# Kernel optimization log

Measured on AMD Instinct MI355X. Metric: run time of the kernel, lower is better.

Reference implementation:

```python
import jax, jax.numpy as jnp
import numpy as np

NUM_GROUPS = 32
EPS = 1e-6
HEAD = 8


def group_norm(x, gamma, beta):
    # x: (b, c, h, w); normalize per group of channels over (c/g, h, w)
    b, c, h, w = x.shape
    g = NUM_GROUPS
    xg = x.reshape(b, g, c // g, h, w)
    mean = xg.mean(axis=(2, 3, 4), keepdims=True)
    var = xg.var(axis=(2, 3, 4), keepdims=True)
    xn = ((xg - mean) * jax.lax.rsqrt(var + EPS)).reshape(b, c, h, w)
    return xn * gamma[None, :, None, None] + beta[None, :, None, None]


def setup_inputs() -> dict:
    key = jax.random.key(0)
    ks = jax.random.split(key, 6)
    b, c, h, w = 8, 512, 64, 64
    sd = 1.0 / np.sqrt(c)
    return {
        "x": jax.random.normal(ks[0], (b, c, h, w), jnp.float32),
        "gamma": jnp.ones((c,), jnp.float32),
        "beta": jnp.zeros((c,), jnp.float32),
        "Wq": jax.random.normal(ks[1], (c, c), jnp.float32) * sd,
        "Wk": jax.random.normal(ks[2], (c, c), jnp.float32) * sd,
        "Wv": jax.random.normal(ks[3], (c, c), jnp.float32) * sd,
        "Wp": jax.random.normal(ks[4], (c, c), jnp.float32) * sd,
        "bp": jnp.zeros((c,), jnp.float32),
    }


def reference(x, gamma, beta, Wq, Wk, Wv, Wp, bp):
    b, c, h, w = x.shape
    hd = c // HEAD
    scale = jnp.sqrt(jnp.float32(hd))  # NOTE: original MULTIPLIES by sqrt(d)
    xn = group_norm(x, gamma, beta)            # (b, c, h, w)
    x_ = xn.reshape(b, c, h * w).transpose(0, 2, 1)  # (b, n, c), n = h*w
    # torch Linear: y = x @ W.T
    Q = (x_ @ Wq.T).reshape(b, h * w, HEAD, hd)
    K = (x_ @ Wk.T).reshape(b, h * w, HEAD, hd)
    V = (x_ @ Wv.T).reshape(b, h * w, HEAD, hd)
    # einsum 'bhid,bhjd->bhij' with axes (b, n, head, hd): per-position head gram
    dots = jnp.einsum('bnid,bnjd->bnij', Q, K) * scale  # (b, n, head, head)
    att = jax.nn.softmax(dots, axis=1)  # softmax over the SPATIAL axis (dim=1)
    out = jnp.einsum('bnij,bnjd->bnid', att, V).reshape(b, h * w, c)
    out = out @ Wp.T + bp  # dropout is identity at inference
    return out.transpose(0, 2, 1).reshape(b, c, h, w) + xn  # residual adds normed x
```

## Files before the change

kernel.cpp:

```cpp
#include <hip/hip_runtime.h>
#include <stdint.h>

typedef unsigned short ushort_t;
typedef _Float16 half8 __attribute__((ext_vector_type(8)));
typedef float f32x4 __attribute__((ext_vector_type(4)));

#define GLOBAL_AS __attribute__((address_space(1)))
#define LDS_AS    __attribute__((address_space(3)))

__device__ __forceinline__ float bf2f(ushort_t u) {
    union { unsigned i; float f; } v; v.i = ((unsigned)u) << 16; return v.f;
}
__device__ __forceinline__ ushort_t f2h(float f) {
    union { _Float16 h; ushort_t u; } v; v.h = (_Float16)f; return v.u;
}
__device__ __forceinline__ float h2f(ushort_t u) {
    union { _Float16 h; ushort_t u; } v; v.u = u; return (float)v.h;
}

__device__ __forceinline__ void async16(const void* g, void* l) {
    __builtin_amdgcn_global_load_lds((const GLOBAL_AS uint32_t*)g,
                                     (LDS_AS uint32_t*)l, 16, 0, 0);
}

__device__ __forceinline__ int is_bf16_in(const uint32_t* g32) {
    return *g32 == 0x3F803F80u;
}

__global__ __launch_bounds__(256) void vecconv(const void* g, const void* be, const void* bp,
                                               float* gcan, float* bcan, float* bpcan,
                                               const uint32_t* g32) {
    int t = threadIdx.x + blockIdx.x * 256;
    if (is_bf16_in(g32)) {
        gcan[t]  = bf2f(((const ushort_t*)g)[t]);
        bcan[t]  = bf2f(((const ushort_t*)be)[t]);
        bpcan[t] = bf2f(((const ushort_t*)bp)[t]);
    } else {
        gcan[t]  = ((const float*)g)[t];
        bcan[t]  = ((const float*)be)[t];
        bpcan[t] = ((const float*)bp)[t];
    }
}

__global__ __launch_bounds__(256) void wconv(const void* Wq, const void* Wk,
                                             const void* Wv, const void* Wp,
                                             ushort_t* Wh, const uint32_t* g32) {
    const void* src = (blockIdx.y == 0) ? Wq : (blockIdx.y == 1) ? Wk
                    : (blockIdx.y == 2) ? Wv : Wp;
    ushort_t* dst = Wh + (size_t)blockIdx.y * 262144;
    const int e0 = blockIdx.x * 2048 + threadIdx.x * 8;
    ushort_t o[8];
    if (is_bf16_in(g32)) {
        uint4 u = *(const uint4*)((const ushort_t*)src + e0);
        const ushort_t* e = (const ushort_t*)&u;
#pragma unroll
        for (int j = 0; j < 8; ++j) o[j] = f2h(bf2f(e[j]));
    } else {
        float4 a = *(const float4*)((const float*)src + e0);
        float4 b = *(const float4*)((const float*)src + e0 + 4);
        o[0] = f2h(a.x); o[1] = f2h(a.y); o[2] = f2h(a.z); o[3] = f2h(a.w);
        o[4] = f2h(b.x); o[5] = f2h(b.y); o[6] = f2h(b.z); o[7] = f2h(b.w);
    }
    *(uint4*)(dst + e0) = *(const uint4*)o;
}

__global__ __launch_bounds__(256) void gn_part(const void* xv, float* __restrict__ psums,
                                               const uint32_t* g32) {
    const int bx = blockIdx.x, t = threadIdx.x;
    const size_t base = (size_t)(bx >> 3) * 65536 + (size_t)(bx & 7) * 8192;
    float s = 0.f, sq = 0.f;
    if (is_bf16_in(g32)) {
        const ushort_t* p = (const ushort_t*)xv + base;
        for (int i = 0; i < 4; ++i) {
            uint4 u = ((const uint4*)p)[t + 256 * i];
            const ushort_t* e = (const ushort_t*)&u;
#pragma unroll
            for (int j = 0; j < 8; ++j) { float f = bf2f(e[j]); s += f; sq += f * f; }
        }
    } else {
        const float* p = (const float*)xv + base;
        for (int i = 0; i < 8; ++i) {
            float4 v = ((const float4*)p)[t + 256 * i];
            s += v.x + v.y + v.z + v.w;
            sq += v.x * v.x + v.y * v.y + v.z * v.z + v.w * v.w;
        }
    }
    __shared__ float ls[256], lq[256];
    ls[t] = s; lq[t] = sq;
    __syncthreads();
    for (int off = 128; off > 0; off >>= 1) {
        if (t < off) { ls[t] += ls[t + off]; lq[t] += lq[t + off]; }
        __syncthreads();
    }
    if (t == 0) { psums[bx * 2] = ls[0]; psums[bx * 2 + 1] = lq[0]; }
}

__global__ __launch_bounds__(256) void gn_fin(const float* __restrict__ psums,
                                              float* __restrict__ stats) {
    const int t = threadIdx.x;
    float s = 0.f, q = 0.f;
#pragma unroll
    for (int k = 0; k < 8; ++k) { s += psums[(t * 8 + k) * 2]; q += psums[(t * 8 + k) * 2 + 1]; }
    float mean = s * (1.f / 65536.f);
    float var  = q * (1.f / 65536.f) - mean * mean;
    stats[t * 2 + 0] = mean;
    stats[t * 2 + 1] = rsqrtf(fmaxf(var, 0.f) + 1e-6f);
}

__global__ __launch_bounds__(256) void gn_apply_t(const void* xv,
                                                  const float* __restrict__ gcan,
                                                  const float* __restrict__ bcan,
                                                  const float* __restrict__ stats,
                                                  ushort_t* __restrict__ xnt,
                                                  const uint32_t* g32) {
    const int nt = blockIdx.x;
    const int ct = blockIdx.y;
    const int b  = blockIdx.z;
    const int t  = threadIdx.x;
    const int c0 = ct * 64, n0 = nt * 64;
    __shared__ __align__(16) ushort_t tile[64 * 80];
    if (is_bf16_in(g32)) {
        const ushort_t* x = (const ushort_t*)xv;
#pragma unroll
        for (int p = 0; p < 2; ++p) {
            int u = p * 256 + t;
            int cc = u >> 3, nc = u & 7;
            int c = c0 + cc;
            uint4 raw = *(const uint4*)(x + ((size_t)(b * 512 + c)) * 4096 + n0 + nc * 8);
            float mean = stats[(b * 32 + (c >> 4)) * 2 + 0];
            float rstd = stats[(b * 32 + (c >> 4)) * 2 + 1];
            float sc = rstd * gcan[c];
            float sh = bcan[c] - mean * sc;
            const ushort_t* e = (const ushort_t*)&raw;
#pragma unroll
            for (int j = 0; j < 8; ++j)
                tile[(nc * 8 + j) * 80 + cc] = f2h(bf2f(e[j]) * sc + sh);
        }
    } else {
        const float* x = (const float*)xv;
#pragma unroll
        for (int p = 0; p < 4; ++p) {
            int u = p * 256 + t;
            int cc = u >> 4, nc = u & 15;
            int c = c0 + cc;
            float4 raw = *(const float4*)(x + ((size_t)(b * 512 + c)) * 4096 + n0 + nc * 4);
            float mean = stats[(b * 32 + (c >> 4)) * 2 + 0];
            float rstd = stats[(b * 32 + (c >> 4)) * 2 + 1];
            float sc = rstd * gcan[c];
            float sh = bcan[c] - mean * sc;
            tile[(nc * 4 + 0) * 80 + cc] = f2h(raw.x * sc + sh);
            tile[(nc * 4 + 1) * 80 + cc] = f2h(raw.y * sc + sh);
            tile[(nc * 4 + 2) * 80 + cc] = f2h(raw.z * sc + sh);
            tile[(nc * 4 + 3) * 80 + cc] = f2h(raw.w * sc + sh);
        }
    }
    __syncthreads();
#pragma unroll
    for (int p = 0; p < 2; ++p) {
        int u = p * 256 + t;
        int nn = u >> 3, cchunk = u & 7;
        uint4 o = *(const uint4*)(tile + nn * 80 + cchunk * 8);
        *(uint4*)(xnt + ((size_t)(b * 4096 + n0 + nn)) * 512 + c0 + cchunk * 8) = o;
    }
}

__device__ __forceinline__ void gemm128_core(const ushort_t* __restrict__ A,
                                             const ushort_t* __restrict__ B,
                                             int m0, int n0, int K, f32x4 acc[4][4]) {
    __shared__ __align__(16) ushort_t As[128 * 32];
    __shared__ __align__(16) ushort_t Bs[128 * 32];
    const int t = threadIdx.x;
    const int l = t & 63;
    const int w = t >> 6;
    const int wm = (w >> 1) * 64, wn = (w & 1) * 64;
    const int lr = l & 15, q = l >> 4;
    f32x4 zero = {0.f, 0.f, 0.f, 0.f};
#pragma unroll
    for (int mi = 0; mi < 4; ++mi)
#pragma unroll
        for (int ni = 0; ni < 4; ++ni) acc[mi][ni] = zero;

    for (int kt = 0; kt < K; kt += 32) {
        __syncthreads();
#pragma unroll
        for (int p = 0; p < 2; ++p) {
            int s = p * 256 + t;
            int r = s >> 2, kc = s & 3;
            async16(A + (size_t)(m0 + r) * K + kt + kc * 8, (char*)As + p * 4096 + w * 1024);
            async16(B + (size_t)(n0 + r) * K + kt + kc * 8, (char*)Bs + p * 4096 + w * 1024);
        }
        __syncthreads();
        half8 af[4], bf[4];
#pragma unroll
        for (int mi = 0; mi < 4; ++mi)
            af[mi] = *(const half8*)(As + (wm + mi * 16 + lr) * 32 + q * 8);
#pragma unroll
        for (int ni = 0; ni < 4; ++ni)
            bf[ni] = *(const half8*)(Bs + (wn + ni * 16 + lr) * 32 + q * 8);
#pragma unroll
        for (int mi = 0; mi < 4; ++mi)
#pragma unroll
            for (int ni = 0; ni < 4; ++ni)
                acc[mi][ni] = __builtin_amdgcn_mfma_f32_16x16x32_f16(af[mi], bf[ni],
                                                                    acc[mi][ni], 0, 0, 0);
    }
}

__global__ __launch_bounds__(256) void gemm_qkv(const ushort_t* __restrict__ xnt,
                                                const ushort_t* __restrict__ Wh,
                                                ushort_t* __restrict__ Qo,
                                                ushort_t* __restrict__ Ko,
                                                ushort_t* __restrict__ Vo) {
    const int n0 = blockIdx.x * 128;
    const int m0 = blockIdx.y * 128;
    const int z  = blockIdx.z;
    const ushort_t* B = Wh + (size_t)z * 262144;
    ushort_t* C = (z == 0) ? Qo : (z == 1) ? Ko : Vo;
    f32x4 acc[4][4];
    gemm128_core(xnt, B, m0, n0, 512, acc);
    const int t = threadIdx.x, l = t & 63, w = t >> 6;
    const int wm = (w >> 1) * 64, wn = (w & 1) * 64;
    const int col = l & 15, q = l >> 4;
#pragma unroll
    for (int mi = 0; mi < 4; ++mi)
#pragma unroll
        for (int ni = 0; ni < 4; ++ni)
#pragma unroll
            for (int r = 0; r < 4; ++r) {
                int row = wm + mi * 16 + q * 4 + r;
                int cc  = wn + ni * 16 + col;
                C[(size_t)(m0 + row) * 512 + n0 + cc] = f2h(acc[mi][ni][r]);
            }
}

__global__ __launch_bounds__(256) void dots_k(const ushort_t* __restrict__ Q,
                                              const ushort_t* __restrict__ K,
                                              float* __restrict__ dots) {
    const int t = threadIdx.x, l = t & 63, w = t >> 6;
    const int gp0 = blockIdx.x * 8 + w * 2;
    const int m = l & 15, q = l >> 4;
    const size_t base = (size_t)(gp0 + (m >> 3)) * 512 + (m & 7) * 64 + q * 8;
    half8 a0 = *(const half8*)(Q + base);
    half8 a1 = *(const half8*)(Q + base + 32);
    half8 b0 = *(const half8*)(K + base);
    half8 b1 = *(const half8*)(K + base + 32);
    f32x4 acc = {0.f, 0.f, 0.f, 0.f};
    acc = __builtin_amdgcn_mfma_f32_16x16x32_f16(a0, b0, acc, 0, 0, 0);
    acc = __builtin_amdgcn_mfma_f32_16x16x32_f16(a1, b1, acc, 0, 0, 0);
    const int col = l & 15;
#pragma unroll
    for (int r = 0; r < 4; ++r) {
        int row = q * 4 + r;
        if (row < 8 && col < 8)
            dots[(size_t)gp0 * 64 + row * 8 + col] = acc[r] * 8.0f;
        if (row >= 8 && col >= 8)
            dots[(size_t)(gp0 + 1) * 64 + (row - 8) * 8 + (col - 8)] = acc[r] * 8.0f;
    }
}

__global__ __launch_bounds__(256) void smax_part(const float* __restrict__ dots,
                                                 float* __restrict__ pmax,
                                                 float* __restrict__ psum) {
    const int chunk = blockIdx.x;
    const int t = threadIdx.x;
    const int ij = t & 63, sub = t >> 6;
    const size_t base = ((size_t)chunk * 128 + sub * 32) * 64 + ij;
    float v[32];
    float m = -1e30f;
#pragma unroll
    for (int r = 0; r < 32; ++r) { v[r] = dots[base + (size_t)r * 64]; m = fmaxf(m, v[r]); }
    __shared__ float lm[4][64];
    __shared__ float lsum[4][64];
    lm[sub][ij] = m;
    __syncthreads();
    float cm = fmaxf(fmaxf(lm[0][ij], lm[1][ij]), fmaxf(lm[2][ij], lm[3][ij]));
    float s = 0.f;
#pragma unroll
    for (int r = 0; r < 32; ++r) s += __expf(v[r] - cm);
    lsum[sub][ij] = s;
    __syncthreads();
    if (sub == 0) {
        pmax[chunk * 64 + ij] = cm;
        psum[chunk * 64 + ij] = lsum[0][ij] + lsum[1][ij] + lsum[2][ij] + lsum[3][ij];
    }
}

__global__ __launch_bounds__(64) void smax_final(const float* __restrict__ pmax,
                                                 const float* __restrict__ psum,
                                                 float* __restrict__ Mout,
                                                 float* __restrict__ Sinv) {
    const int b = blockIdx.x;
    const int ij = threadIdx.x;
    float pm[32];
    float M = -1e30f;
#pragma unroll
    for (int c = 0; c < 32; ++c) { pm[c] = pmax[(b * 32 + c) * 64 + ij]; M = fmaxf(M, pm[c]); }
    float S = 0.f;
#pragma unroll
    for (int c = 0; c < 32; ++c) S += psum[(b * 32 + c) * 64 + ij] * __expf(pm[c] - M);
    Mout[b * 64 + ij] = M;
    Sinv[b * 64 + ij] = 1.f / S;
}

__global__ __launch_bounds__(256) void attn_apply(const float* __restrict__ dots,
                                                  const float* __restrict__ Mbuf,
                                                  const float* __restrict__ Sinv,
                                                  const ushort_t* __restrict__ V,
                                                  ushort_t* __restrict__ P) {
    const int t = threadIdx.x, l = t & 63, w = t >> 6;
    const int gp = blockIdx.x * 4 + w;
    const int b = gp >> 12;
    __shared__ float att[4][64];
    __shared__ __align__(16) ushort_t vb[4][512];
    float d = dots[(size_t)gp * 64 + l];
    att[w][l] = __expf(d - Mbuf[b * 64 + l]) * Sinv[b * 64 + l];
    *(uint4*)(&vb[w][l * 8]) = *(const uint4*)(V + (size_t)gp * 512 + l * 8);
    __syncthreads();
    const int i = l >> 3, dc = l & 7;
    float o[8] = {0, 0, 0, 0, 0, 0, 0, 0};
#pragma unroll
    for (int j = 0; j < 8; ++j) {
        float a = att[w][i * 8 + j];
        uint4 vv = *(const uint4*)(&vb[w][j * 64 + dc * 8]);
        const ushort_t* ve = (const ushort_t*)&vv;
#pragma unroll
        for (int k2 = 0; k2 < 8; ++k2) o[k2] += a * h2f(ve[k2]);
    }
    ushort_t ou[8];
#pragma unroll
    for (int k2 = 0; k2 < 8; ++k2) ou[k2] = f2h(o[k2]);
    *(uint4*)(P + (size_t)gp * 512 + l * 8) = *(const uint4*)ou;
}

__global__ __launch_bounds__(256) void gemm_out(const ushort_t* __restrict__ Wph,
                                                const ushort_t* __restrict__ P,
                                                const void* xv,
                                                const float* __restrict__ gcan,
                                                const float* __restrict__ bcan,
                                                const float* __restrict__ bpcan,
                                                const float* __restrict__ stats,
                                                float* __restrict__ out,
                                                const uint32_t* g32) {
    const int n0 = blockIdx.x * 128;
    const int o0 = blockIdx.y * 128;
    const int b  = blockIdx.z;
    f32x4 acc[4][4];
    gemm128_core(Wph, P + (size_t)b * 4096 * 512, o0, n0, 512, acc);
    const int t = threadIdx.x, l = t & 63, w = t >> 6;
    const int wm = (w >> 1) * 64, wn = (w & 1) * 64;
    const int col = l & 15, q = l >> 4;
    const int isbf = is_bf16_in(g32);
    const ushort_t* xbf = (const ushort_t*)xv;
    const float*    xf  = (const float*)xv;
#pragma unroll
    for (int mi = 0; mi < 4; ++mi) {
#pragma unroll
        for (int r = 0; r < 4; ++r) {
            int o = o0 + wm + mi * 16 + q * 4 + r;
            float mean = stats[(b * 32 + (o >> 4)) * 2 + 0];
            float rstd = stats[(b * 32 + (o >> 4)) * 2 + 1];
            float sc = rstd * gcan[o];
            float sh = bcan[o] - mean * sc;
            float bias = bpcan[o];
#pragma unroll
            for (int ni = 0; ni < 4; ++ni) {
                int n = n0 + wn + ni * 16 + col;
                size_t idx = ((size_t)(b * 512 + o)) * 4096 + n;
                float xval = isbf ? bf2f(xbf[idx]) : xf[idx];
                float xn = xval * sc + sh;
                out[idx] = acc[mi][ni][r] + bias + xn;
            }
        }
    }
}

extern "C" void kernel_launch(void* const* d_in, const int* in_sizes, int n_in,
                              void* d_out, int out_size, void* d_ws, size_t ws_size,
                              hipStream_t stream) {
    const void* x     = d_in[0];
    const void* gamma = d_in[1];
    const void* beta  = d_in[2];
    const void* Wq    = d_in[3];
    const void* Wk    = d_in[4];
    const void* Wv    = d_in[5];
    const void* Wp    = d_in[6];
    const void* bp    = d_in[7];
    const uint32_t* g32 = (const uint32_t*)gamma;
    float* out = (float*)d_out;

    char* ws = (char*)d_ws;
    const size_t SZ = 33554432;
    ushort_t* xnt = (ushort_t*)(ws);
    ushort_t* Qh  = (ushort_t*)(ws + 1 * SZ);
    ushort_t* Kh  = (ushort_t*)(ws + 2 * SZ);
    ushort_t* Vh  = (ushort_t*)(ws + 3 * SZ);
    float* dots   = (float*)(ws + 4 * SZ);
    ushort_t* Wh  = (ushort_t*)(ws + 4 * SZ + 8388608);
    char* tail    = ws + 4 * SZ + 8388608 + 2097152;
    float* gcan   = (float*)(tail);
    float* bcan   = gcan + 512;
    float* bpcan  = bcan + 512;
    float* stats  = bpcan + 512;
    float* psums  = stats + 512;
    float* pmax   = psums + 4096;
    float* psumS  = pmax + 16384;
    float* Mbuf   = psumS + 16384;
    float* Sinv   = Mbuf + 512;
    ushort_t* Pb  = xnt;

    vecconv   <<<2, 256, 0, stream>>>(gamma, beta, bp, gcan, bcan, bpcan, g32);
    wconv     <<<dim3(128, 4), 256, 0, stream>>>(Wq, Wk, Wv, Wp, Wh, g32);
    gn_part   <<<2048, 256, 0, stream>>>(x, psums, g32);
    gn_fin    <<<1, 256, 0, stream>>>(psums, stats);
    gn_apply_t<<<dim3(64, 8, 8), 256, 0, stream>>>(x, gcan, bcan, stats, xnt, g32);
    gemm_qkv  <<<dim3(4, 256, 3), 256, 0, stream>>>(xnt, Wh, Qh, Kh, Vh);
    dots_k    <<<4096, 256, 0, stream>>>(Qh, Kh, dots);
    smax_part <<<256, 256, 0, stream>>>(dots, pmax, psumS);
    smax_final<<<8, 64, 0, stream>>>(pmax, psumS, Mbuf, Sinv);
    attn_apply<<<8192, 256, 0, stream>>>(dots, Mbuf, Sinv, Vh, Pb);
    gemm_out  <<<dim3(32, 4, 8), 256, 0, stream>>>(Wh + 3 * 262144, Pb, x,
                                                   gcan, bcan, bpcan, stats, out, g32);
}
```

Baseline: 320.5 us.

## Cache fp16 normalized x for residual and remap GEMM blocks per XCD

gn_apply_t now also writes an fp16 copy of the normalized input in channel-major layout. gemm_out reads that copy for the residual instead of re-reading fp32 x and recomputing the group-norm affine, which halves residual read bytes at the cost of an extra 32MB write. Both GEMMs switch to a 1D grid whose block index is remapped so that blocks landing on the same XCD share A/B tiles, aiming to improve L2 reuse. Using fp16 for the residual adds rounding error.

```diff
diff --git a/kernel.cpp b/kernel.cpp
--- a/kernel.cpp
+++ b/kernel.cpp
@@ -112,6 +112,7 @@
                                                   const float* __restrict__ bcan,
                                                   const float* __restrict__ stats,
                                                   ushort_t* __restrict__ xnt,
+                                                  ushort_t* __restrict__ xnc,
                                                   const uint32_t* g32) {
     const int nt = blockIdx.x;
     const int ct = blockIdx.y;
@@ -126,15 +127,20 @@
             int u = p * 256 + t;
             int cc = u >> 3, nc = u & 7;
             int c = c0 + cc;
-            uint4 raw = *(const uint4*)(x + ((size_t)(b * 512 + c)) * 4096 + n0 + nc * 8);
+            size_t gidx = ((size_t)(b * 512 + c)) * 4096 + n0 + nc * 8;
+            uint4 raw = *(const uint4*)(x + gidx);
             float mean = stats[(b * 32 + (c >> 4)) * 2 + 0];
             float rstd = stats[(b * 32 + (c >> 4)) * 2 + 1];
             float sc = rstd * gcan[c];
             float sh = bcan[c] - mean * sc;
             const ushort_t* e = (const ushort_t*)&raw;
-#pragma unroll
-            for (int j = 0; j < 8; ++j)
-                tile[(nc * 8 + j) * 80 + cc] = f2h(bf2f(e[j]) * sc + sh);
+            ushort_t hv[8];
+#pragma unroll
+            for (int j = 0; j < 8; ++j) {
+                hv[j] = f2h(bf2f(e[j]) * sc + sh);
+                tile[(nc * 8 + j) * 80 + cc] = hv[j];
+            }
+            *(uint4*)(xnc + gidx) = *(const uint4*)hv;
         }
     } else {
         const float* x = (const float*)xv;
@@ -143,15 +149,20 @@
             int u = p * 256 + t;
             int cc = u >> 4, nc = u & 15;
             int c = c0 + cc;
-            float4 raw = *(const float4*)(x + ((size_t)(b * 512 + c)) * 4096 + n0 + nc * 4);
+            size_t gidx = ((size_t)(b * 512 + c)) * 4096 + n0 + nc * 4;
+            float4 raw = *(const float4*)(x + gidx);
             float mean = stats[(b * 32 + (c >> 4)) * 2 + 0];
             float rstd = stats[(b * 32 + (c >> 4)) * 2 + 1];
             float sc = rstd * gcan[c];
             float sh = bcan[c] - mean * sc;
-            tile[(nc * 4 + 0) * 80 + cc] = f2h(raw.x * sc + sh);
-            tile[(nc * 4 + 1) * 80 + cc] = f2h(raw.y * sc + sh);
-            tile[(nc * 4 + 2) * 80 + cc] = f2h(raw.z * sc + sh);
-            tile[(nc * 4 + 3) * 80 + cc] = f2h(raw.w * sc + sh);
+            ushort_t hv[4];
+            hv[0] = f2h(raw.x * sc + sh);
+            hv[1] = f2h(raw.y * sc + sh);
+            hv[2] = f2h(raw.z * sc + sh);
+            hv[3] = f2h(raw.w * sc + sh);
+#pragma unroll
+            for (int j = 0; j < 4; ++j) tile[(nc * 4 + j) * 80 + cc] = hv[j];
+            *(uint2*)(xnc + gidx) = *(const uint2*)hv;
         }
     }
     __syncthreads();
@@ -211,9 +222,12 @@
                                                 ushort_t* __restrict__ Qo,
                                                 ushort_t* __restrict__ Ko,
                                                 ushort_t* __restrict__ Vo) {
-    const int n0 = blockIdx.x * 128;
-    const int m0 = blockIdx.y * 128;
-    const int z  = blockIdx.z;
+    const int id = blockIdx.x;
+    const int xcd = id & 7, s = id >> 3;
+    const int mloc = s / 12, r = s % 12;
+    const int m0 = (xcd * 32 + mloc) * 128;
+    const int n0 = (r & 3) * 128;
+    const int z  = r >> 2;
     const ushort_t* B = Wh + (size_t)z * 262144;
     ushort_t* C = (z == 0) ? Qo : (z == 1) ? Ko : Vo;
     f32x4 acc[4][4];
@@ -226,10 +240,10 @@
 #pragma unroll
         for (int ni = 0; ni < 4; ++ni)
 #pragma unroll
-            for (int r = 0; r < 4; ++r) {
-                int row = wm + mi * 16 + q * 4 + r;
+            for (int rr = 0; rr < 4; ++rr) {
+                int row = wm + mi * 16 + q * 4 + rr;
                 int cc  = wn + ni * 16 + col;
-                C[(size_t)(m0 + row) * 512 + n0 + cc] = f2h(acc[mi][ni][r]);
+                C[(size_t)(m0 + row) * 512 + n0 + cc] = f2h(acc[mi][ni][rr]);
             }
 }
 
@@ -334,41 +348,31 @@
 
 __global__ __launch_bounds__(256) void gemm_out(const ushort_t* __restrict__ Wph,
                                                 const ushort_t* __restrict__ P,
-                                                const void* xv,
-                                                const float* __restrict__ gcan,
-                                                const float* __restrict__ bcan,
+                                                const ushort_t* __restrict__ xnc,
                                                 const float* __restrict__ bpcan,
-                                                const float* __restrict__ stats,
-                                                float* __restrict__ out,
-                                                const uint32_t* g32) {
-    const int n0 = blockIdx.x * 128;
-    const int o0 = blockIdx.y * 128;
-    const int b  = blockIdx.z;
+                                                float* __restrict__ out) {
+    const int id = blockIdx.x;
+    const int xcd = id & 7, s = id >> 3;
+    const int pair = xcd * 32 + (s >> 2);
+    const int o0 = (s & 3) * 128;
+    const int b  = pair >> 5;
+    const int n0 = (pair & 31) * 128;
     f32x4 acc[4][4];
     gemm128_core(Wph, P + (size_t)b * 4096 * 512, o0, n0, 512, acc);
     const int t = threadIdx.x, l = t & 63, w = t >> 6;
     const int wm = (w >> 1) * 64, wn = (w & 1) * 64;
     const int col = l & 15, q = l >> 4;
-    const int isbf = is_bf16_in(g32);
-    const ushort_t* xbf = (const ushort_t*)xv;
-    const float*    xf  = (const float*)xv;
 #pragma unroll
     for (int mi = 0; mi < 4; ++mi) {
 #pragma unroll
         for (int r = 0; r < 4; ++r) {
             int o = o0 + wm + mi * 16 + q * 4 + r;
-            float mean = stats[(b * 32 + (o >> 4)) * 2 + 0];
-            float rstd = stats[(b * 32 + (o >> 4)) * 2 + 1];
-            float sc = rstd * gcan[o];
-            float sh = bcan[o] - mean * sc;
             float bias = bpcan[o];
 #pragma unroll
             for (int ni = 0; ni < 4; ++ni) {
                 int n = n0 + wn + ni * 16 + col;
                 size_t idx = ((size_t)(b * 512 + o)) * 4096 + n;
-                float xval = isbf ? bf2f(xbf[idx]) : xf[idx];
-                float xn = xval * sc + sh;
-                out[idx] = acc[mi][ni][r] + bias + xn;
+                out[idx] = acc[mi][ni][r] + bias + h2f(xnc[idx]);
             }
         }
     }
@@ -396,7 +400,8 @@
     ushort_t* Vh  = (ushort_t*)(ws + 3 * SZ);
     float* dots   = (float*)(ws + 4 * SZ);
     ushort_t* Wh  = (ushort_t*)(ws + 4 * SZ + 8388608);
-    char* tail    = ws + 4 * SZ + 8388608 + 2097152;
+    ushort_t* xnc = (ushort_t*)(ws + 4 * SZ + 8388608 + 2097152);
+    char* tail    = ws + 4 * SZ + 8388608 + 2097152 + SZ;
     float* gcan   = (float*)(tail);
     float* bcan   = gcan + 512;
     float* bpcan  = bcan + 512;
@@ -412,12 +417,11 @@
     wconv     <<<dim3(128, 4), 256, 0, stream>>>(Wq, Wk, Wv, Wp, Wh, g32);
     gn_part   <<<2048, 256, 0, stream>>>(x, psums, g32);
     gn_fin    <<<1, 256, 0, stream>>>(psums, stats);
-    gn_apply_t<<<dim3(64, 8, 8), 256, 0, stream>>>(x, gcan, bcan, stats, xnt, g32);
-    gemm_qkv  <<<dim3(4, 256, 3), 256, 0, stream>>>(xnt, Wh, Qh, Kh, Vh);
+    gn_apply_t<<<dim3(64, 8, 8), 256, 0, stream>>>(x, gcan, bcan, stats, xnt, xnc, g32);
+    gemm_qkv  <<<3072, 256, 0, stream>>>(xnt, Wh, Qh, Kh, Vh);
     dots_k    <<<4096, 256, 0, stream>>>(Qh, Kh, dots);
     smax_part <<<256, 256, 0, stream>>>(dots, pmax, psumS);
     smax_final<<<8, 64, 0, stream>>>(pmax, psumS, Mbuf, Sinv);
     attn_apply<<<8192, 256, 0, stream>>>(dots, Mbuf, Sinv, Vh, Pb);
-    gemm_out  <<<dim3(32, 4, 8), 256, 0, stream>>>(Wh + 3 * 262144, Pb, x,
-                                                   gcan, bcan, bpcan, stats, out, g32);
-}
+    gemm_out  <<<1024, 256, 0, stream>>>(Wh + 3 * 262144, Pb, xnc, bpcan, out);
+}
```

After: 294.2 us. 1.09x faster.
